# Optimization experiments

Measured on AMD Instinct MI355X. Metric: run time of the kernel, lower is better.

Reference implementation:

```python
import jax, jax.numpy as jnp
import numpy as np

N_NODES = 30000
NEG_SLOPE = 0.2  # PyG GATConv default leaky_relu slope


def gat_conv(x, src, dst, W, a_src, a_dst, b, num_nodes, concat):
    """One PyG-style GATConv layer (add_self_loops already applied to src/dst).
    x: [N, F_in]; W: [F_in, H*C]; a_src, a_dst: [H, C]; b: [H*C] or [C].
    """
    H, C = a_src.shape
    h = (x @ W).reshape(num_nodes, H, C)                     # [N, H, C]
    alpha_src = jnp.einsum('nhc,hc->nh', h, a_src)           # [N, H]
    alpha_dst = jnp.einsum('nhc,hc->nh', h, a_dst)           # [N, H]
    e = jax.nn.leaky_relu(alpha_src[src] + alpha_dst[dst], NEG_SLOPE)  # [E, H]
    # scatter-softmax over incoming edges of each dst node
    e_max = jax.ops.segment_max(e, dst, num_segments=num_nodes)        # [N, H]
    e_exp = jnp.exp(e - e_max[dst])                                    # [E, H]
    denom = jax.ops.segment_sum(e_exp, dst, num_segments=num_nodes)    # [N, H]
    alpha = e_exp / denom[dst]                                         # [E, H]
    msg = h[src] * alpha[:, :, None]                                   # [E, H, C]
    out = jax.ops.segment_sum(msg, dst, num_segments=num_nodes)        # [N, H, C]
    out = out.reshape(num_nodes, H * C) if concat else out.mean(axis=1)
    return out + b


def _glorot(key, shape):
    fan = sum(shape[:2]) if len(shape) > 1 else shape[0] * 2
    return jax.random.normal(key, shape, dtype=jnp.float32) * np.sqrt(2.0 / fan)


def setup_inputs() -> dict:
    key = jax.random.key(0)
    ks = jax.random.split(key, 16)
    n, f_in, heads = N_NODES, 256, 4
    x = jax.random.normal(ks[0], (n, f_in), dtype=jnp.float32)
    edge_index = jax.random.randint(ks[1], (2, 480000), 0, n, dtype=jnp.int64)
    inp = {
        'x': x, 'edge_index': edge_index,
        'W1': _glorot(ks[2], (f_in, heads * 128)),
        'a1s': _glorot(ks[3], (heads, 128)), 'a1d': _glorot(ks[4], (heads, 128)),
        'b1': jnp.zeros((heads * 128,), jnp.float32),
        'W2': _glorot(ks[5], (heads * 128, heads * 128)),
        'a2s': _glorot(ks[6], (heads, 128)), 'a2d': _glorot(ks[7], (heads, 128)),
        'b2': jnp.zeros((heads * 128,), jnp.float32),
        'W3': _glorot(ks[8], (heads * 128, heads * 64)),
        'a3s': _glorot(ks[9], (heads, 64)), 'a3d': _glorot(ks[10], (heads, 64)),
        'b3': jnp.zeros((heads * 64,), jnp.float32),
        # conv4: 256 -> 64, 1 head, mean (concat=False)
        'W4': _glorot(ks[11], (heads * 64, 64)),
        'a4s': _glorot(ks[12], (1, 64)), 'a4d': _glorot(ks[13], (1, 64)),
        'b4': jnp.zeros((64,), jnp.float32),
    }
    return inp


def reference(x, edge_index, W1, a1s, a1d, b1, W2, a2s, a2d, b2,
              W3, a3s, a3d, b3, W4, a4s, a4d, b4):
    n = x.shape[0]
    # PyG GATConv default add_self_loops=True
    loops = jnp.arange(n, dtype=edge_index.dtype)
    src = jnp.concatenate([edge_index[0], loops])
    dst = jnp.concatenate([edge_index[1], loops])
    h = jax.nn.relu(gat_conv(x, src, dst, W1, a1s, a1d, b1, n, True))
    h = jax.nn.relu(gat_conv(h, src, dst, W2, a2s, a2d, b2, n, True))
    h = jax.nn.relu(gat_conv(h, src, dst, W3, a3s, a3d, b3, n, True))
    h = jax.nn.relu(gat_conv(h, src, dst, W4, a4s, a4d, b4, n, False))
    return h
```

## Files before the change

kernel.cpp:

```cpp
#include <hip/hip_runtime.h>
#include <hip/hip_fp16.h>
#include <math.h>


typedef __attribute__((ext_vector_type(8))) __bf16 bf16x8;
typedef __attribute__((ext_vector_type(4))) float floatx4;
typedef __attribute__((ext_vector_type(8))) unsigned short usv8;
typedef __attribute__((ext_vector_type(4))) unsigned short usv4;

__device__ __forceinline__ unsigned short f2bf(float f) {
    unsigned int u = __float_as_uint(f);
    u += 0x7fff + ((u >> 16) & 1);
    return (unsigned short)(u >> 16);
}
__device__ __forceinline__ float bf2f(unsigned short u) {
    return __uint_as_float(((unsigned int)u) << 16);
}
__device__ __forceinline__ float lrelu(float e) {
    return (e > 0.f) ? e : 0.2f * e;
}
__device__ __forceinline__ void gload16(const void* g, void* l) {
    __builtin_amdgcn_global_load_lds(
        (const __attribute__((address_space(1))) void*)g,
        (__attribute__((address_space(3))) void*)l, 16, 0, 0);
}

static __global__ void zero_int(int* __restrict__ p, int n) {
    int i = blockIdx.x * blockDim.x + threadIdx.x;
    if (i < n) p[i] = 0;
}
static __global__ void zero_float(float* __restrict__ p, int n) {
    int i = blockIdx.x * blockDim.x + threadIdx.x;
    if (i < n) p[i] = 0.f;
}

static __global__ void hist_kernel(const int* __restrict__ ei, int e0, int n_nodes,
                                   int* __restrict__ counts) {
    int e = blockIdx.x * blockDim.x + threadIdx.x;
    int et = e0 + n_nodes;
    if (e >= et) return;
    int d = (e < e0) ? ei[e0 + e] : (e - e0);
    atomicAdd(&counts[d], 1);
}

static __global__ void scan_kernel(const int* __restrict__ counts,
                                   int* __restrict__ row_ptr,
                                   int* __restrict__ cursor, int n) {
    __shared__ int sdata[1024];
    int tid = threadIdx.x;
    int per = (n + 1023) / 1024;
    int start = tid * per;
    int stop = min(start + per, n);
    if (start > n) start = n;
    int s = 0;
    for (int i = start; i < stop; i++) s += counts[i];
    sdata[tid] = s;
    __syncthreads();
    for (int off = 1; off < 1024; off <<= 1) {
        int t = (tid >= off) ? sdata[tid - off] : 0;
        __syncthreads();
        sdata[tid] += t;
        __syncthreads();
    }
    int run = sdata[tid] - s;
    for (int i = start; i < stop; i++) {
        row_ptr[i] = run;
        cursor[i] = run;
        run += counts[i];
    }
    if (stop == n) row_ptr[n] = run;
}

static __global__ void scatter_kernel(const int* __restrict__ ei, int e0, int n_nodes,
                                      int* __restrict__ cursor,
                                      int* __restrict__ src_sorted) {
    int e = blockIdx.x * blockDim.x + threadIdx.x;
    int et = e0 + n_nodes;
    if (e >= et) return;
    int s, d;
    if (e < e0) { s = ei[e]; d = ei[e0 + e]; } else { s = e - e0; d = s; }
    int pos = atomicAdd(&cursor[d], 1);
    src_sorted[pos] = s;
}

static __global__ void convA_kernel(const float* __restrict__ X,
                                    unsigned short* __restrict__ A, int M, int K) {
    int idx = blockIdx.x * 256 + threadIdx.x;
    if (idx >= M * K) return;
    int m = idx / K, k = idx % K;
    float v = X[idx];
    unsigned short hi = f2bf(v);
    size_t base = (size_t)m * (2 * K);
    A[base + k] = hi;
    A[base + K + k] = f2bf(v - bf2f(hi));
}

__device__ __forceinline__ void convW_one(const float* W, unsigned short* BT,
                                          int idx, int K, int N) {
    int n = idx / K, k = idx % K;
    float v = (n < N) ? W[(size_t)k * N + n] : 0.f;
    unsigned short hi = f2bf(v);
    unsigned short lo = f2bf(v - bf2f(hi));
    size_t base = (size_t)n * (3 * K);
    BT[base + k] = hi;
    BT[base + K + k] = hi;
    BT[base + 2 * K + k] = lo;
}

static __global__ void convW_all(const float* __restrict__ W1, unsigned short* __restrict__ BT1,
                                 const float* __restrict__ W2, unsigned short* __restrict__ BT2,
                                 const float* __restrict__ W3, unsigned short* __restrict__ BT3,
                                 const float* __restrict__ W4, unsigned short* __restrict__ BT4) {
    int idx = blockIdx.x * 256 + threadIdx.x;
    if (idx < 131072) { convW_one(W1, BT1, idx, 256, 512); return; }
    idx -= 131072;
    if (idx < 262144) { convW_one(W2, BT2, idx, 512, 512); return; }
    idx -= 262144;
    if (idx < 131072) { convW_one(W3, BT3, idx, 512, 256); return; }
    idx -= 131072;
    if (idx < 32768)  { convW_one(W4, BT4, idx, 256, 64); }
}

#define BM 128
#define BN 128
#define BKK 64

template <bool CF16>
__launch_bounds__(256)
static __global__ void gemm_mfma(const unsigned short* __restrict__ A,
                                 const unsigned short* __restrict__ B,
                                 void* __restrict__ Cv, int M, int K, int N,
                                 const float* __restrict__ asv,
                                 const float* __restrict__ adv,
                                 float* __restrict__ as_out,
                                 float* __restrict__ ad_out,
                                 int Hh, int Cc) {
    __shared__ __align__(16) unsigned short lds[2 * BM * BKK];
    const int tid  = threadIdx.x;
    const int lane = tid & 63;
    const int wave = tid >> 6;
    const int r0 = blockIdx.y * BM;
    const int c0 = blockIdx.x * BN;
    const int wm = (wave >> 1) * 64;
    const int wn = (wave & 1) * 64;
    const int q   = lane >> 4;
    const int m16 = lane & 15;

    floatx4 acc[4][4];
#pragma unroll
    for (int i = 0; i < 4; i++)
#pragma unroll
        for (int j = 0; j < 4; j++) acc[i][j] = {0.f, 0.f, 0.f, 0.f};

    const size_t sA = (size_t)(2 * K);
    const size_t sB = (size_t)(3 * K);
    char* ldsb = (char*)lds;

#pragma unroll 1
    for (int seg = 0; seg < 3; seg++) {
        const int aoff = (seg == 1) ? K : 0;
        const int boff = seg * K;
#pragma unroll 1
        for (int k0 = 0; k0 < K; k0 += BKK) {
            __syncthreads();
#pragma unroll
            for (int c = 0; c < 4; c++) {
                int slot = c * 256 + tid;
                int row = slot >> 3;
                int gc  = (slot & 7) ^ (row & 7);
                gload16(A + (size_t)(r0 + row) * sA + aoff + k0 + gc * 8,
                        ldsb + slot * 16);
                gload16(B + (size_t)(c0 + row) * sB + boff + k0 + gc * 8,
                        ldsb + 16384 + slot * 16);
            }
            __syncthreads();
#pragma unroll
            for (int ks = 0; ks < 2; ks++) {
                bf16x8 af[4], bfr[4];
#pragma unroll
                for (int i = 0; i < 4; i++) {
                    int row = wm + i * 16 + m16;
                    int ch  = (q + ks * 4) ^ (row & 7);
                    af[i] = *(const bf16x8*)(ldsb + (row * 8 + ch) * 16);
                }
#pragma unroll
                for (int j = 0; j < 4; j++) {
                    int row = wn + j * 16 + m16;
                    int ch  = (q + ks * 4) ^ (row & 7);
                    bfr[j] = *(const bf16x8*)(ldsb + 16384 + (row * 8 + ch) * 16);
                }
#pragma unroll
                for (int i = 0; i < 4; i++)
#pragma unroll
                    for (int j = 0; j < 4; j++)
                        acc[i][j] = __builtin_amdgcn_mfma_f32_16x16x32_bf16(
                            af[i], bfr[j], acc[i][j], 0, 0, 0);
            }
        }
    }
#pragma unroll
    for (int i = 0; i < 4; i++)
#pragma unroll
        for (int j = 0; j < 4; j++)
#pragma unroll
            for (int r = 0; r < 4; r++) {
                int row = r0 + wm + i * 16 + q * 4 + r;
                int col = c0 + wn + j * 16 + m16;
                if (row < M && col < N) {
                    if constexpr (CF16) {
                        __half* C = (__half*)Cv;
                        C[(size_t)row * N + col] = __float2half(acc[i][j][r]);
                    } else {
                        float* C = (float*)Cv;
                        C[(size_t)row * N + col] = acc[i][j][r];
                    }
                }
            }
    if (c0 + wn < N) {
        int head = (c0 + wn) / Cc;
#pragma unroll
        for (int i = 0; i < 4; i++)
#pragma unroll
            for (int r = 0; r < 4; r++) {
                float ps = 0.f, pd = 0.f;
#pragma unroll
                for (int j = 0; j < 4; j++) {
                    int c = c0 + wn + j * 16 + m16;
                    float v = acc[i][j][r];
                    ps = fmaf(v, asv[c], ps);
                    pd = fmaf(v, adv[c], pd);
                }
#pragma unroll
                for (int off = 1; off < 16; off <<= 1) {
                    ps += __shfl_xor(ps, off);
                    pd += __shfl_xor(pd, off);
                }
                if (m16 == 0) {
                    int row = r0 + wm + i * 16 + q * 4 + r;
                    if (row < M) {
                        atomicAdd(&as_out[(size_t)row * Hh + head], ps);
                        atomicAdd(&ad_out[(size_t)row * Hh + head], pd);
                    }
                }
            }
    }
}

template <int R, bool HF16>
__device__ __forceinline__ void accum_row(const void* hptr, size_t off, float w,
                                          float* acc) {
    if constexpr (HF16) {
        const __half* p = (const __half*)hptr + off;
        if constexpr (R == 8) {
            float4 raw = *(const float4*)p;
            const __half2* hp = (const __half2*)&raw;
#pragma unroll
            for (int qq = 0; qq < 4; qq++) {
                float2 f = __half22float2(hp[qq]);
                acc[2 * qq + 0] += w * f.x;
                acc[2 * qq + 1] += w * f.y;
            }
        } else if constexpr (R == 4) {
            float2 raw = *(const float2*)p;
            const __half2* hp = (const __half2*)&raw;
#pragma unroll
            for (int qq = 0; qq < 2; qq++) {
                float2 f = __half22float2(hp[qq]);
                acc[2 * qq + 0] += w * f.x;
                acc[2 * qq + 1] += w * f.y;
            }
        } else {
            acc[0] += w * __half2float(*p);
        }
    } else {
        const float* p = (const float*)hptr + off;
        if constexpr (R >= 4) {
#pragma unroll
            for (int qq = 0; qq < R / 4; qq++) {
                float4 v = ((const float4*)p)[qq];
                acc[4 * qq + 0] += w * v.x;
                acc[4 * qq + 1] += w * v.y;
                acc[4 * qq + 2] += w * v.z;
                acc[4 * qq + 3] += w * v.w;
            }
        } else {
#pragma unroll
            for (int r = 0; r < R; r++) acc[r] += w * p[r];
        }
    }
}

template <int H, int C, bool BF16OUT, bool HF16>
__launch_bounds__(256)
static __global__ void agg_kernel(const void* __restrict__ h,
                                  const float* __restrict__ as_arr,
                                  const float* __restrict__ ad_arr,
                                  const int* __restrict__ row_ptr,
                                  const int* __restrict__ src_sorted,
                                  const float* __restrict__ bias,
                                  float* __restrict__ outf,
                                  unsigned short* __restrict__ outb, int n_nodes) {
    constexpr int R = H * C / 64;
    constexpr int G = 64 / H;
    constexpr int K = H * C;
    int wave = threadIdx.x >> 6;
    int lane = threadIdx.x & 63;
    int n = blockIdx.x * 4 + wave;
    if (n >= n_nodes) return;
    int beg = row_ptr[n], end = row_ptr[n + 1];

    float ad_h[H], m_h[H], l_h[H];
#pragma unroll
    for (int hh = 0; hh < H; hh++) {
        ad_h[hh] = ad_arr[(size_t)n * H + hh];
        m_h[hh] = -INFINITY;
        l_h[hh] = 0.f;
    }
    for (int base = beg; base < end; base += 64) {
        int j = base + lane;
        bool ok = j < end;
        float e_h[H];
        if (ok) {
            int s = src_sorted[j];
            if constexpr (H == 4) {
                float4 a = ((const float4*)as_arr)[s];
                e_h[0] = lrelu(a.x + ad_h[0]);
                e_h[1] = lrelu(a.y + ad_h[1]);
                e_h[2] = lrelu(a.z + ad_h[2]);
                e_h[3] = lrelu(a.w + ad_h[3]);
            } else {
                e_h[0] = lrelu(as_arr[s] + ad_h[0]);
            }
        } else {
#pragma unroll
            for (int hh = 0; hh < H; hh++) e_h[hh] = -INFINITY;
        }
#pragma unroll
        for (int hh = 0; hh < H; hh++) {
            float cm = e_h[hh];
#pragma unroll
            for (int off = 1; off < 64; off <<= 1) cm = fmaxf(cm, __shfl_xor(cm, off));
            float newm = fmaxf(m_h[hh], cm);
            float p = ok ? __expf(e_h[hh] - newm) : 0.f;
#pragma unroll
            for (int off = 1; off < 64; off <<= 1) p += __shfl_xor(p, off);
            l_h[hh] = l_h[hh] * __expf(m_h[hh] - newm) + p;
            m_h[hh] = newm;
        }
    }
    int myh = lane / G;
    float mm, adm, inv;
    if constexpr (H == 4) {
        mm  = m_h[0];  mm  = (myh == 1) ? m_h[1] : mm;  mm  = (myh == 2) ? m_h[2] : mm;  mm  = (myh == 3) ? m_h[3] : mm;
        float ll = l_h[0]; ll = (myh == 1) ? l_h[1] : ll; ll = (myh == 2) ? l_h[2] : ll; ll = (myh == 3) ? l_h[3] : ll;
        adm = ad_h[0]; adm = (myh == 1) ? ad_h[1] : adm; adm = (myh == 2) ? ad_h[2] : adm; adm = (myh == 3) ? ad_h[3] : adm;
        inv = 1.f / ll;
    } else {
        mm = m_h[0]; adm = ad_h[0]; inv = 1.f / l_h[0];
    }

    float acc[R];
#pragma unroll
    for (int r = 0; r < R; r++) acc[r] = 0.f;

    int j = beg;
    for (; j + 3 < end; j += 4) {
        int s0 = src_sorted[j];
        int s1 = src_sorted[j + 1];
        int s2 = src_sorted[j + 2];
        int s3 = src_sorted[j + 3];
        float w0 = __expf(lrelu(as_arr[(size_t)s0 * H + myh] + adm) - mm) * inv;
        float w1 = __expf(lrelu(as_arr[(size_t)s1 * H + myh] + adm) - mm) * inv;
        float w2 = __expf(lrelu(as_arr[(size_t)s2 * H + myh] + adm) - mm) * inv;
        float w3 = __expf(lrelu(as_arr[(size_t)s3 * H + myh] + adm) - mm) * inv;
        accum_row<R, HF16>(h, (size_t)s0 * K + lane * R, w0, acc);
        accum_row<R, HF16>(h, (size_t)s1 * K + lane * R, w1, acc);
        accum_row<R, HF16>(h, (size_t)s2 * K + lane * R, w2, acc);
        accum_row<R, HF16>(h, (size_t)s3 * K + lane * R, w3, acc);
    }
    for (; j < end; j++) {
        int s0 = src_sorted[j];
        float w0 = __expf(lrelu(as_arr[(size_t)s0 * H + myh] + adm) - mm) * inv;
        accum_row<R, HF16>(h, (size_t)s0 * K + lane * R, w0, acc);
    }

    float vout[R];
#pragma unroll
    for (int r = 0; r < R; r++)
        vout[r] = fmaxf(acc[r] + bias[lane * R + r], 0.f);

    if constexpr (BF16OUT) {
        unsigned short hi[R], lo[R];
#pragma unroll
        for (int r = 0; r < R; r++) {
            hi[r] = f2bf(vout[r]);
            lo[r] = f2bf(vout[r] - bf2f(hi[r]));
        }
        size_t base = (size_t)n * (2 * K) + lane * R;
        if constexpr (R == 8) {
            usv8 vh = {hi[0], hi[1], hi[2], hi[3], hi[4], hi[5], hi[6], hi[7]};
            usv8 vl = {lo[0], lo[1], lo[2], lo[3], lo[4], lo[5], lo[6], lo[7]};
            *(usv8*)(outb + base) = vh;
            *(usv8*)(outb + base + K) = vl;
        } else if constexpr (R == 4) {
            usv4 vh = {hi[0], hi[1], hi[2], hi[3]};
            usv4 vl = {lo[0], lo[1], lo[2], lo[3]};
            *(usv4*)(outb + base) = vh;
            *(usv4*)(outb + base + K) = vl;
        } else {
#pragma unroll
            for (int r = 0; r < R; r++) {
                outb[base + r] = hi[r];
                outb[base + K + r] = lo[r];
            }
        }
    } else {
#pragma unroll
        for (int r = 0; r < R; r++)
            outf[(size_t)n * K + lane * R + r] = vout[r];
    }
}


static inline size_t align_up(size_t x) { return (x + 255) & ~(size_t)255; }

extern "C" void kernel_launch(void* const* d_in, const int* in_sizes, int n_in,
                              void* d_out, int out_size, void* d_ws, size_t ws_size,
                              hipStream_t stream) {
    const float* x   = (const float*)d_in[0];
    const int*   ei  = (const int*)d_in[1];
    const float* W1  = (const float*)d_in[2];
    const float* a1s = (const float*)d_in[3];
    const float* a1d = (const float*)d_in[4];
    const float* b1  = (const float*)d_in[5];
    const float* W2  = (const float*)d_in[6];
    const float* a2s = (const float*)d_in[7];
    const float* a2d = (const float*)d_in[8];
    const float* b2  = (const float*)d_in[9];
    const float* W3  = (const float*)d_in[10];
    const float* a3s = (const float*)d_in[11];
    const float* a3d = (const float*)d_in[12];
    const float* b3  = (const float*)d_in[13];
    const float* W4  = (const float*)d_in[14];
    const float* a4s = (const float*)d_in[15];
    const float* a4d = (const float*)d_in[16];
    const float* b4  = (const float*)d_in[17];

    const int n  = in_sizes[0] / 256;
    const int e0 = in_sizes[1] / 2;
    const int et = e0 + n;
    const int Mpad = ((n + 127) / 128) * 128;

    char* w = (char*)d_ws;
    unsigned short* slotA = (unsigned short*)w;  w += align_up((size_t)Mpad * 1024 * 2);
    char* hbuf = (char*)w;                       w += align_up((size_t)n * 512 * 4);
    unsigned short* WT1 = (unsigned short*)w;    w += align_up((size_t)512 * 768 * 2);
    unsigned short* WT2 = (unsigned short*)w;    w += align_up((size_t)512 * 1536 * 2);
    unsigned short* WT3 = (unsigned short*)w;    w += align_up((size_t)256 * 1536 * 2);
    unsigned short* WT4 = (unsigned short*)w;    w += align_up((size_t)128 * 768 * 2);
    float* as_b = (float*)w;                     w += align_up((size_t)n * 4 * 4);
    float* ad_b = (float*)w;                     w += align_up((size_t)n * 4 * 4);
    int* row_ptr = (int*)w;                      w += align_up((size_t)(n + 1) * 4);
    int* counts  = (int*)w;                      w += align_up((size_t)n * 4);
    int* cursor  = (int*)w;                      w += align_up((size_t)n * 4);
    int* src_sorted = (int*)w;                   w += align_up((size_t)et * 4);
    (void)ws_size;

    dim3 blk(256);
    int nodeblocks = (n + 3) / 4;

    zero_int<<<(n + 255) / 256, 256, 0, stream>>>(counts, n);
    hist_kernel<<<(et + 255) / 256, 256, 0, stream>>>(ei, e0, n, counts);
    scan_kernel<<<1, 1024, 0, stream>>>(counts, row_ptr, cursor, n);
    scatter_kernel<<<(et + 255) / 256, 256, 0, stream>>>(ei, e0, n, cursor, src_sorted);

    convA_kernel<<<((n * 256) + 255) / 256, blk, 0, stream>>>(x, slotA, n, 256);
    convW_all<<<(557056 + 255) / 256, blk, 0, stream>>>(W1, WT1, W2, WT2, W3, WT3, W4, WT4);

    const int mblocks = Mpad / 128;
    const int zeroN = n * 8;

    zero_float<<<(zeroN + 255) / 256, blk, 0, stream>>>(as_b, zeroN);
    gemm_mfma<true><<<dim3(4, mblocks), blk, 0, stream>>>(slotA, WT1, hbuf, n, 256, 512,
                                                          a1s, a1d, as_b, ad_b, 4, 128);
    agg_kernel<4, 128, true, true><<<nodeblocks, blk, 0, stream>>>(hbuf, as_b, ad_b, row_ptr, src_sorted, b1, nullptr, slotA, n);

    zero_float<<<(zeroN + 255) / 256, blk, 0, stream>>>(as_b, zeroN);
    gemm_mfma<true><<<dim3(4, mblocks), blk, 0, stream>>>(slotA, WT2, hbuf, n, 512, 512,
                                                          a2s, a2d, as_b, ad_b, 4, 128);
    agg_kernel<4, 128, true, true><<<nodeblocks, blk, 0, stream>>>(hbuf, as_b, ad_b, row_ptr, src_sorted, b2, nullptr, slotA, n);

    zero_float<<<(zeroN + 255) / 256, blk, 0, stream>>>(as_b, zeroN);
    gemm_mfma<true><<<dim3(2, mblocks), blk, 0, stream>>>(slotA, WT3, hbuf, n, 512, 256,
                                                          a3s, a3d, as_b, ad_b, 4, 64);
    agg_kernel<4, 64, true, true><<<nodeblocks, blk, 0, stream>>>(hbuf, as_b, ad_b, row_ptr, src_sorted, b3, nullptr, slotA, n);

    zero_float<<<(zeroN + 255) / 256, blk, 0, stream>>>(as_b, zeroN);
    gemm_mfma<false><<<dim3(1, mblocks), blk, 0, stream>>>(slotA, WT4, hbuf, n, 256, 64,
                                                           a4s, a4d, as_b, ad_b, 1, 64);
    agg_kernel<1, 64, false, false><<<nodeblocks, blk, 0, stream>>>(hbuf, as_b, ad_b, row_ptr, src_sorted, b4, (float*)d_out, nullptr, n);
}
```

Measured before the change: 673.4 us.

## Fuse split-bf16 GEMM passes into one K loop with grouped tile order

The three-segment split-bf16 GEMM (hi*hi, lo*hi, hi*lo) becomes a single K loop. Each step loads the hi and lo tiles of both A and B into LDS and issues three MFMAs per fragment pair, so A and B are read from global memory once instead of three times. The weight layout shrinks to two copies (hi and lo), the launch becomes 1D with 8-row band swizzling for L2 reuse, and launch bounds ask for 2 blocks per CU. Doubling LDS to 64KB and holding more fragments in registers may lower occupancy, and the last layer's h is now stored as fp16 instead of fp32, which costs precision.

```diff
diff --git a/kernel.cpp b/kernel.cpp
--- a/kernel.cpp
+++ b/kernel.cpp
@@ -100,11 +100,9 @@
     int n = idx / K, k = idx % K;
     float v = (n < N) ? W[(size_t)k * N + n] : 0.f;
     unsigned short hi = f2bf(v);
-    unsigned short lo = f2bf(v - bf2f(hi));
-    size_t base = (size_t)n * (3 * K);
+    size_t base = (size_t)n * (2 * K);
     BT[base + k] = hi;
-    BT[base + K + k] = hi;
-    BT[base + 2 * K + k] = lo;
+    BT[base + K + k] = f2bf(v - bf2f(hi));
 }
 
 static __global__ void convW_all(const float* __restrict__ W1, unsigned short* __restrict__ BT1,
@@ -125,22 +123,30 @@
 #define BN 128
 #define BKK 64
 
-template <bool CF16>
-__launch_bounds__(256)
+__launch_bounds__(256, 2)
 static __global__ void gemm_mfma(const unsigned short* __restrict__ A,
                                  const unsigned short* __restrict__ B,
-                                 void* __restrict__ Cv, int M, int K, int N,
+                                 __half* __restrict__ C, int M, int K, int N,
+                                 int xcols, int mblocks,
                                  const float* __restrict__ asv,
                                  const float* __restrict__ adv,
                                  float* __restrict__ as_out,
                                  float* __restrict__ ad_out,
                                  int Hh, int Cc) {
-    __shared__ __align__(16) unsigned short lds[2 * BM * BKK];
+    __shared__ __align__(16) unsigned short lds[4 * BM * BKK];
     const int tid  = threadIdx.x;
     const int lane = tid & 63;
     const int wave = tid >> 6;
-    const int r0 = blockIdx.y * BM;
-    const int c0 = blockIdx.x * BN;
+
+    const int id = blockIdx.x;
+    const int band = id / (8 * xcols);
+    const int rem = id - band * 8 * xcols;
+    const int band_rows = min(8, mblocks - band * 8);
+    const int ry = rem % band_rows;
+    const int rx = rem / band_rows;
+    const int r0 = (band * 8 + ry) * BM;
+    const int c0 = rx * BN;
+
     const int wm = (wave >> 1) * 64;
     const int wn = (wave & 1) * 64;
     const int q   = lane >> 4;
@@ -153,49 +159,55 @@
         for (int j = 0; j < 4; j++) acc[i][j] = {0.f, 0.f, 0.f, 0.f};
 
     const size_t sA = (size_t)(2 * K);
-    const size_t sB = (size_t)(3 * K);
+    const size_t sB = (size_t)(2 * K);
     char* ldsb = (char*)lds;
 
 #pragma unroll 1
-    for (int seg = 0; seg < 3; seg++) {
-        const int aoff = (seg == 1) ? K : 0;
-        const int boff = seg * K;
-#pragma unroll 1
-        for (int k0 = 0; k0 < K; k0 += BKK) {
-            __syncthreads();
-#pragma unroll
-            for (int c = 0; c < 4; c++) {
-                int slot = c * 256 + tid;
-                int row = slot >> 3;
-                int gc  = (slot & 7) ^ (row & 7);
-                gload16(A + (size_t)(r0 + row) * sA + aoff + k0 + gc * 8,
-                        ldsb + slot * 16);
-                gload16(B + (size_t)(c0 + row) * sB + boff + k0 + gc * 8,
-                        ldsb + 16384 + slot * 16);
-            }
-            __syncthreads();
-#pragma unroll
-            for (int ks = 0; ks < 2; ks++) {
-                bf16x8 af[4], bfr[4];
-#pragma unroll
-                for (int i = 0; i < 4; i++) {
-                    int row = wm + i * 16 + m16;
-                    int ch  = (q + ks * 4) ^ (row & 7);
-                    af[i] = *(const bf16x8*)(ldsb + (row * 8 + ch) * 16);
+    for (int k0 = 0; k0 < K; k0 += BKK) {
+        __syncthreads();
+#pragma unroll
+        for (int c = 0; c < 4; c++) {
+            int slot = c * 256 + tid;
+            int row = slot >> 3;
+            int gc  = (slot & 7) ^ (row & 7);
+            const unsigned short* Ab = A + (size_t)(r0 + row) * sA + k0 + gc * 8;
+            const unsigned short* Bb = B + (size_t)(c0 + row) * sB + k0 + gc * 8;
+            gload16(Ab,     ldsb + slot * 16);
+            gload16(Ab + K, ldsb + 16384 + slot * 16);
+            gload16(Bb,     ldsb + 32768 + slot * 16);
+            gload16(Bb + K, ldsb + 49152 + slot * 16);
+        }
+        __syncthreads();
+#pragma unroll
+        for (int ks = 0; ks < 2; ks++) {
+            bf16x8 ah[4], al[4], bh[4], bl[4];
+#pragma unroll
+            for (int i = 0; i < 4; i++) {
+                int row = wm + i * 16 + m16;
+                int ch  = (q + ks * 4) ^ (row & 7);
+                int off = (row * 8 + ch) * 16;
+                ah[i] = *(const bf16x8*)(ldsb + off);
+                al[i] = *(const bf16x8*)(ldsb + 16384 + off);
+            }
+#pragma unroll
+            for (int j = 0; j < 4; j++) {
+                int row = wn + j * 16 + m16;
+                int ch  = (q + ks * 4) ^ (row & 7);
+                int off = (row * 8 + ch) * 16;
+                bh[j] = *(const bf16x8*)(ldsb + 32768 + off);
+                bl[j] = *(const bf16x8*)(ldsb + 49152 + off);
+            }
+#pragma unroll
+            for (int i = 0; i < 4; i++)
+#pragma unroll
+                for (int j = 0; j < 4; j++) {
+                    acc[i][j] = __builtin_amdgcn_mfma_f32_16x16x32_bf16(
+                        ah[i], bh[j], acc[i][j], 0, 0, 0);
+                    acc[i][j] = __builtin_amdgcn_mfma_f32_16x16x32_bf16(
+                        al[i], bh[j], acc[i][j], 0, 0, 0);
+                    acc[i][j] = __builtin_amdgcn_mfma_f32_16x16x32_bf16(
+                        ah[i], bl[j], acc[i][j], 0, 0, 0);
                 }
-#pragma unroll
-                for (int j = 0; j < 4; j++) {
-                    int row = wn + j * 16 + m16;
-                    int ch  = (q + ks * 4) ^ (row & 7);
-                    bfr[j] = *(const bf16x8*)(ldsb + 16384 + (row * 8 + ch) * 16);
-                }
-#pragma unroll
-                for (int i = 0; i < 4; i++)
-#pragma unroll
-                    for (int j = 0; j < 4; j++)
-                        acc[i][j] = __builtin_amdgcn_mfma_f32_16x16x32_bf16(
-                            af[i], bfr[j], acc[i][j], 0, 0, 0);
-            }
         }
     }
 #pragma unroll
@@ -206,15 +218,8 @@
             for (int r = 0; r < 4; r++) {
                 int row = r0 + wm + i * 16 + q * 4 + r;
                 int col = c0 + wn + j * 16 + m16;
-                if (row < M && col < N) {
-                    if constexpr (CF16) {
-                        __half* C = (__half*)Cv;
-                        C[(size_t)row * N + col] = __float2half(acc[i][j][r]);
-                    } else {
-                        float* C = (float*)Cv;
-                        C[(size_t)row * N + col] = acc[i][j][r];
-                    }
-                }
+                if (row < M && col < N)
+                    C[(size_t)row * N + col] = __float2half(acc[i][j][r]);
             }
     if (c0 + wn < N) {
         int head = (c0 + wn) / Cc;
@@ -246,53 +251,36 @@
     }
 }
 
-template <int R, bool HF16>
-__device__ __forceinline__ void accum_row(const void* hptr, size_t off, float w,
+template <int R>
+__device__ __forceinline__ void accum_row(const __half* hptr, size_t off, float w,
                                           float* acc) {
-    if constexpr (HF16) {
-        const __half* p = (const __half*)hptr + off;
-        if constexpr (R == 8) {
-            float4 raw = *(const float4*)p;
-            const __half2* hp = (const __half2*)&raw;
-#pragma unroll
-            for (int qq = 0; qq < 4; qq++) {
-                float2 f = __half22float2(hp[qq]);
-                acc[2 * qq + 0] += w * f.x;
-                acc[2 * qq + 1] += w * f.y;
-            }
-        } else if constexpr (R == 4) {
-            float2 raw = *(const float2*)p;
-            const __half2* hp = (const __half2*)&raw;
-#pragma unroll
-            for (int qq = 0; qq < 2; qq++) {
-                float2 f = __half22float2(hp[qq]);
-                acc[2 * qq + 0] += w * f.x;
-                acc[2 * qq + 1] += w * f.y;
-            }
-        } else {
-            acc[0] += w * __half2float(*p);
+    const __half* p = hptr + off;
+    if constexpr (R == 8) {
+        float4 raw = *(const float4*)p;
+        const __half2* hp = (const __half2*)&raw;
+#pragma unroll
+        for (int qq = 0; qq < 4; qq++) {
+            float2 f = __half22float2(hp[qq]);
+            acc[2 * qq + 0] += w * f.x;
+            acc[2 * qq + 1] += w * f.y;
+        }
+    } else if constexpr (R == 4) {
+        float2 raw = *(const float2*)p;
+        const __half2* hp = (const __half2*)&raw;
+#pragma unroll
+        for (int qq = 0; qq < 2; qq++) {
+            float2 f = __half22float2(hp[qq]);
+            acc[2 * qq + 0] += w * f.x;
+            acc[2 * qq + 1] += w * f.y;
         }
     } else {
-        const float* p = (const float*)hptr + off;
-        if constexpr (R >= 4) {
-#pragma unroll
-            for (int qq = 0; qq < R / 4; qq++) {
-                float4 v = ((const float4*)p)[qq];
-                acc[4 * qq + 0] += w * v.x;
-                acc[4 * qq + 1] += w * v.y;
-                acc[4 * qq + 2] += w * v.z;
-                acc[4 * qq + 3] += w * v.w;
-            }
-        } else {
-#pragma unroll
-            for (int r = 0; r < R; r++) acc[r] += w * p[r];
-        }
-    }
-}
-
-template <int H, int C, bool BF16OUT, bool HF16>
+        acc[0] += w * __half2float(*p);
+    }
+}
+
+template <int H, int C, bool BF16OUT>
 __launch_bounds__(256)
-static __global__ void agg_kernel(const void* __restrict__ h,
+static __global__ void agg_kernel(const __half* __restrict__ h,
                                   const float* __restrict__ as_arr,
                                   const float* __restrict__ ad_arr,
                                   const int* __restrict__ row_ptr,
@@ -373,15 +361,15 @@
         float w1 = __expf(lrelu(as_arr[(size_t)s1 * H + myh] + adm) - mm) * inv;
         float w2 = __expf(lrelu(as_arr[(size_t)s2 * H + myh] + adm) - mm) * inv;
         float w3 = __expf(lrelu(as_arr[(size_t)s3 * H + myh] + adm) - mm) * inv;
-        accum_row<R, HF16>(h, (size_t)s0 * K + lane * R, w0, acc);
-        accum_row<R, HF16>(h, (size_t)s1 * K + lane * R, w1, acc);
-        accum_row<R, HF16>(h, (size_t)s2 * K + lane * R, w2, acc);
-        accum_row<R, HF16>(h, (size_t)s3 * K + lane * R, w3, acc);
+        accum_row<R>(h, (size_t)s0 * K + lane * R, w0, acc);
+        accum_row<R>(h, (size_t)s1 * K + lane * R, w1, acc);
+        accum_row<R>(h, (size_t)s2 * K + lane * R, w2, acc);
+        accum_row<R>(h, (size_t)s3 * K + lane * R, w3, acc);
     }
     for (; j < end; j++) {
         int s0 = src_sorted[j];
         float w0 = __expf(lrelu(as_arr[(size_t)s0 * H + myh] + adm) - mm) * inv;
-        accum_row<R, HF16>(h, (size_t)s0 * K + lane * R, w0, acc);
+        accum_row<R>(h, (size_t)s0 * K + lane * R, w0, acc);
     }
 
     float vout[R];
@@ -453,11 +441,11 @@
 
     char* w = (char*)d_ws;
     unsigned short* slotA = (unsigned short*)w;  w += align_up((size_t)Mpad * 1024 * 2);
-    char* hbuf = (char*)w;                       w += align_up((size_t)n * 512 * 4);
-    unsigned short* WT1 = (unsigned short*)w;    w += align_up((size_t)512 * 768 * 2);
-    unsigned short* WT2 = (unsigned short*)w;    w += align_up((size_t)512 * 1536 * 2);
-    unsigned short* WT3 = (unsigned short*)w;    w += align_up((size_t)256 * 1536 * 2);
-    unsigned short* WT4 = (unsigned short*)w;    w += align_up((size_t)128 * 768 * 2);
+    __half* hbuf = (__half*)w;                   w += align_up((size_t)n * 512 * 4);
+    unsigned short* WT1 = (unsigned short*)w;    w += align_up((size_t)512 * 512 * 2);
+    unsigned short* WT2 = (unsigned short*)w;    w += align_up((size_t)512 * 1024 * 2);
+    unsigned short* WT3 = (unsigned short*)w;    w += align_up((size_t)256 * 1024 * 2);
+    unsigned short* WT4 = (unsigned short*)w;    w += align_up((size_t)128 * 512 * 2);
     float* as_b = (float*)w;                     w += align_up((size_t)n * 4 * 4);
     float* ad_b = (float*)w;                     w += align_up((size_t)n * 4 * 4);
     int* row_ptr = (int*)w;                      w += align_up((size_t)(n + 1) * 4);
@@ -481,22 +469,22 @@
     const int zeroN = n * 8;
 
     zero_float<<<(zeroN + 255) / 256, blk, 0, stream>>>(as_b, zeroN);
-    gemm_mfma<true><<<dim3(4, mblocks), blk, 0, stream>>>(slotA, WT1, hbuf, n, 256, 512,
-                                                          a1s, a1d, as_b, ad_b, 4, 128);
-    agg_kernel<4, 128, true, true><<<nodeblocks, blk, 0, stream>>>(hbuf, as_b, ad_b, row_ptr, src_sorted, b1, nullptr, slotA, n);
+    gemm_mfma<<<dim3(4 * mblocks), blk, 0, stream>>>(slotA, WT1, hbuf, n, 256, 512, 4, mblocks,
+                                                     a1s, a1d, as_b, ad_b, 4, 128);
+    agg_kernel<4, 128, true><<<nodeblocks, blk, 0, stream>>>(hbuf, as_b, ad_b, row_ptr, src_sorted, b1, nullptr, slotA, n);
 
     zero_float<<<(zeroN + 255) / 256, blk, 0, stream>>>(as_b, zeroN);
-    gemm_mfma<true><<<dim3(4, mblocks), blk, 0, stream>>>(slotA, WT2, hbuf, n, 512, 512,
-                                                          a2s, a2d, as_b, ad_b, 4, 128);
-    agg_kernel<4, 128, true, true><<<nodeblocks, blk, 0, stream>>>(hbuf, as_b, ad_b, row_ptr, src_sorted, b2, nullptr, slotA, n);
+    gemm_mfma<<<dim3(4 * mblocks), blk, 0, stream>>>(slotA, WT2, hbuf, n, 512, 512, 4, mblocks,
+                                                     a2s, a2d, as_b, ad_b, 4, 128);
+    agg_kernel<4, 128, true><<<nodeblocks, blk, 0, stream>>>(hbuf, as_b, ad_b, row_ptr, src_sorted, b2, nullptr, slotA, n);
 
     zero_float<<<(zeroN + 255) / 256, blk, 0, stream>>>(as_b, zeroN);
-    gemm_mfma<true><<<dim3(2, mblocks), blk, 0, stream>>>(slotA, WT3, hbuf, n, 512, 256,
-                                                          a3s, a3d, as_b, ad_b, 4, 64);
-    agg_kernel<4, 64, true, true><<<nodeblocks, blk, 0, stream>>>(hbuf, as_b, ad_b, row_ptr, src_sorted, b3, nullptr, slotA, n);
+    gemm_mfma<<<dim3(2 * mblocks), blk, 0, stream>>>(slotA, WT3, hbuf, n, 512, 256, 2, mblocks,
+                                                     a3s, a3d, as_b, ad_b, 4, 64);
+    agg_kernel<4, 64, true><<<nodeblocks, blk, 0, stream>>>(hbuf, as_b, ad_b, row_ptr, src_sorted, b3, nullptr, slotA, n);
 
     zero_float<<<(zeroN + 255) / 256, blk, 0, stream>>>(as_b, zeroN);
-    gemm_mfma<false><<<dim3(1, mblocks), blk, 0, stream>>>(slotA, WT4, hbuf, n, 256, 64,
-                                                           a4s, a4d, as_b, ad_b, 1, 64);
-    agg_kernel<1, 64, false, false><<<nodeblocks, blk, 0, stream>>>(hbuf, as_b, ad_b, row_ptr, src_sorted, b4, (float*)d_out, nullptr, n);
-}
+    gemm_mfma<<<dim3(1 * mblocks), blk, 0, stream>>>(slotA, WT4, hbuf, n, 256, 64, 1, mblocks,
+                                                     a4s, a4d, as_b, ad_b, 1, 64);
+    agg_kernel<1, 64, false><<<nodeblocks, blk, 0, stream>>>(hbuf, as_b, ad_b, row_ptr, src_sorted, b4, (float*)d_out, nullptr, n);
+}
```

Result: faster. 641.0 us (-4.8%).
